# Optimization experiments

Hardware: AMD Instinct MI355X
Metric: run time of the kernel (lower is better)

The kernel has to match this reference:

```python
import jax, jax.numpy as jnp
import numpy as np

H = 768      # hidden_size
NH = 12      # num_heads
HD = H // NH # head_dim = 64


def setup_inputs() -> dict:
    key = jax.random.key(0)
    k1, k2, k3 = jax.random.split(key, 3)
    x = jax.random.normal(k1, (4, 2048, H), dtype=jnp.float32)
    # nn.Linear weights are [out, in]; we store transposed [in, out] for x @ W
    w_qkv = jax.random.normal(k2, (H, 3 * H), dtype=jnp.float32) * (1.0 / np.sqrt(H))
    w_out = jax.random.normal(k3, (H, H), dtype=jnp.float32) * (1.0 / np.sqrt(H))
    return {"x": x, "w_qkv": w_qkv, "w_out": w_out}


def reference(x, w_qkv, w_out):
    B, S, _ = x.shape
    qkv = (x @ w_qkv).reshape(B, S, 3, NH, HD)
    qkv = jnp.transpose(qkv, (2, 0, 3, 1, 4))  # [3, B, NH, S, HD]
    q, k, v = qkv[0], qkv[1], qkv[2]
    scale = 1.0 / np.sqrt(HD)
    scores = jnp.einsum('bhqd,bhkd->bhqk', q, k) * scale  # [B,NH,S,S]
    causal = jnp.tril(jnp.ones((S, S), dtype=bool))
    scores = jnp.where(causal, scores, jnp.finfo(scores.dtype).min)
    attn = jax.nn.softmax(scores, axis=-1)
    out = jnp.einsum('bhqk,bhkd->bhqd', attn, v)          # [B,NH,S,HD]
    out = jnp.transpose(out, (0, 2, 1, 3)).reshape(B, S, H)
    return out @ w_out
```

## Files before the change

kernel.cpp:

```cpp
#include <hip/hip_runtime.h>
#include <type_traits>

#define S_LEN 2048
#define HID   768
#define NHEAD 12
#define HDIM  64
#define BATCH 4

typedef __attribute__((ext_vector_type(4))) float float4v;
typedef __attribute__((ext_vector_type(8))) short short8;
typedef __attribute__((ext_vector_type(4))) short short4v;
typedef __attribute__((ext_vector_type(2))) int int2v;

__device__ __forceinline__ short f2b(float f) {
  unsigned u = __float_as_uint(f);
  u += 0x7fff + ((u >> 16) & 1);
  return (short)(u >> 16);
}

__device__ __forceinline__ unsigned pkbf(float a, float b) {
#if __has_builtin(__builtin_amdgcn_cvt_pk_bf16_f32)
  typedef __attribute__((ext_vector_type(2))) __bf16 bf2;
  bf2 r = __builtin_amdgcn_cvt_pk_bf16_f32(a, b);
  return *(unsigned*)&r;
#else
  return ((unsigned)(unsigned short)f2b(a)) |
         (((unsigned)(unsigned short)f2b(b)) << 16);
#endif
}

__device__ __forceinline__ float fexp2(float x) {
#if __has_builtin(__builtin_amdgcn_exp2f)
  return __builtin_amdgcn_exp2f(x);
#else
  return __expf(x * 0.69314718056f);
#endif
}

__device__ __forceinline__ void g2l16(const short* g, short* l) {
  __builtin_amdgcn_global_load_lds(
      (const __attribute__((address_space(1))) void*)g,
      (__attribute__((address_space(3))) void*)l, 16, 0, 0);
}

__global__ __launch_bounds__(256) void prepass(const float* __restrict__ x,
                                               const float* __restrict__ w_qkv,
                                               const float* __restrict__ w_out,
                                               short* __restrict__ xb,
                                               short* __restrict__ wqkvT,
                                               short* __restrict__ woutT) {
  __shared__ float tile[64][65];
  const int blk = blockIdx.x;
  if (blk < 3072) {
    int i = blk * 2048 + threadIdx.x * 8;
    float4v a = *(const float4v*)&x[i];
    float4v b = *(const float4v*)&x[i + 4];
    short8 o;
#pragma unroll
    for (int j = 0; j < 4; j++) { o[j] = f2b(a[j]); o[j + 4] = f2b(b[j]); }
    *(short8*)&xb[i] = o;
    return;
  }
  const float* W; short* WT; int N_, scaleN, idx;
  if (blk < 3504) { idx = blk - 3072; W = w_qkv; WT = wqkvT; N_ = 3 * HID; scaleN = HID; }
  else            { idx = blk - 3504; W = w_out; WT = woutT; N_ = HID;     scaleN = 0;  }
  const int nblk = N_ / 64;
  const int n0 = (idx % nblk) * 64, k0 = (idx / nblk) * 64;
  const int tx = threadIdx.x & 63, ty = threadIdx.x >> 6;
#pragma unroll
  for (int r = 0; r < 16; r++) {
    int row = r * 4 + ty;
    tile[row][tx] = W[(size_t)(k0 + row) * N_ + n0 + tx];
  }
  __syncthreads();
#pragma unroll
  for (int r = 0; r < 16; r++) {
    int row = r * 4 + ty;
    float sc = (n0 + row < scaleN) ? 0.18033688011f : 1.0f;
    WT[(size_t)(n0 + row) * HID + k0 + tx] = f2b(tile[tx][row] * sc);
  }
}

template <int OUT>
__global__ __launch_bounds__(256) void gemm_bt(const short* __restrict__ A,
                                               const short* __restrict__ Bt,
                                               float* __restrict__ Cf,
                                               short* __restrict__ Cq,
                                               short* __restrict__ vT,
                                               int M, int N, int K) {
  __shared__ __align__(16) short As[2][128 * 32];
  __shared__ __align__(16) short Bs[2][128 * 32];
  const int tid = threadIdx.x;
  const int w = tid >> 6, lane = tid & 63;
  const int quad = lane >> 4, lm = lane & 15;

  const int gx = gridDim.x;
  const int nwg = gx * gridDim.y;
  int flat = blockIdx.y * gx + blockIdx.x;
  if ((nwg & 7) == 0) flat = (flat & 7) * (nwg >> 3) + (flat >> 3);
  const int m0 = (flat / gx) * 128, n0 = (flat % gx) * 128;
  const int mo = (w & 1) * 64, no = (w >> 1) * 64;

  float4v acc[4][4];
#pragma unroll
  for (int i = 0; i < 4; i++)
#pragma unroll
    for (int j = 0; j < 4; j++) acc[i][j] = (float4v)0.0f;

  const int srow = w * 32 + (lane >> 2);
  const int scol = ((lane & 3) ^ ((lane >> 3) & 3)) * 8;
  const short* Ag = A + (size_t)(m0 + srow) * K + scol;
  const short* Bg = Bt + (size_t)(n0 + srow) * K + scol;

  const int qsw8 = (quad ^ ((lm >> 1) & 3)) * 8;

  for (int kb = 0; kb < K; kb += 64) {
#pragma unroll
    for (int s = 0; s < 2; s++) {
      short* Al = &As[s][(w * 32) * 32];
      short* Bl = &Bs[s][(w * 32) * 32];
      g2l16(Ag + kb + s * 32, Al);
      g2l16(Ag + kb + s * 32 + (size_t)16 * K, Al + 16 * 32);
      g2l16(Bg + kb + s * 32, Bl);
      g2l16(Bg + kb + s * 32 + (size_t)16 * K, Bl + 16 * 32);
    }
    __syncthreads();

#pragma unroll
    for (int s = 0; s < 2; s++) {
      short8 af[4], bf[4];
#pragma unroll
      for (int i = 0; i < 4; i++)
        af[i] = *(const short8*)&As[s][(mo + i * 16 + lm) * 32 + qsw8];
#pragma unroll
      for (int j = 0; j < 4; j++)
        bf[j] = *(const short8*)&Bs[s][(no + j * 16 + lm) * 32 + qsw8];
#pragma unroll
      for (int i = 0; i < 4; i++)
#pragma unroll
        for (int j = 0; j < 4; j++) {
          if constexpr (OUT == 2)
            acc[i][j] = __builtin_amdgcn_mfma_f32_16x16x32_bf16(bf[j], af[i], acc[i][j], 0, 0, 0);
          else
            acc[i][j] = __builtin_amdgcn_mfma_f32_16x16x32_bf16(af[i], bf[j], acc[i][j], 0, 0, 0);
        }
    }
    __syncthreads();
  }

  if constexpr (OUT == 0) {
#pragma unroll
    for (int i = 0; i < 4; i++)
#pragma unroll
      for (int j = 0; j < 4; j++)
#pragma unroll
        for (int r = 0; r < 4; r++)
          Cf[(size_t)(m0 + mo + i * 16 + quad * 4 + r) * N + n0 + no + j * 16 + lm] =
              acc[i][j][r];
  } else if constexpr (OUT == 1) {
#pragma unroll
    for (int i = 0; i < 4; i++)
#pragma unroll
      for (int j = 0; j < 4; j++)
#pragma unroll
        for (int r = 0; r < 4; r++)
          Cq[(size_t)(m0 + mo + i * 16 + quad * 4 + r) * (2 * HID) + n0 + no + j * 16 + lm] =
              f2b(acc[i][j][r]);
  } else {
    const int b = m0 >> 11;
#pragma unroll
    for (int i = 0; i < 4; i++) {
      const int sG = (m0 & 2047) + mo + i * 16 + lm;
#pragma unroll
      for (int j = 0; j < 4; j++) {
#pragma unroll
        for (int r = 0; r < 4; r++) {
          int col = n0 + no + j * 16 + quad * 4 + r;
          int h = col >> 6, d = col & 63;
          vT[((size_t)(b * NHEAD + h) * HDIM + d) * S_LEN + sG] = f2b(acc[i][j][r]);
        }
      }
    }
  }
}

__global__ __launch_bounds__(256) void attn_mfma(const short* __restrict__ qk,
                                                 const short* __restrict__ vT,
                                                 short* __restrict__ attnout) {
  __shared__ __align__(16) short Ks[2][64 * 64];
  __shared__ __align__(16) short Vt[2][64 * 64];
  __shared__ __align__(16) short Ps[4][16 * 64];

  const int tid = threadIdx.x;
  const int w = tid >> 6, lane = tid & 63;
  const int quad = lane >> 4, lm = lane & 15;
  const int bh = blockIdx.x, a = blockIdx.y;
  const int b = bh / NHEAD, h = bh % NHEAD;
  const int qtile[2] = {a, 31 - a};

  short8 aq[2][2];
#pragma unroll
  for (int t = 0; t < 2; t++)
#pragma unroll
    for (int kb = 0; kb < 2; kb++)
      aq[t][kb] = *(const short8*)&qk[(size_t)(b * S_LEN + qtile[t] * 64 + w * 16 + lm) * (2 * HID) +
                                      h * HDIM + kb * 32 + quad * 8];

  const float4v z4 = (float4v)0.0f;
  short8 one8;
#pragma unroll
  for (int j = 0; j < 8; j++) one8[j] = (short)0x3F80;

  const size_t kbase = (size_t)(b * S_LEN) * (2 * HID) + HID + h * HDIM;
  const size_t vbase = (size_t)(b * NHEAD + h) * HDIM * S_LEN;
  const short* kptr[2];
  const short* vptr[2];
#pragma unroll
  for (int i = 0; i < 2; i++) {
    int c = (w * 2 + i) * 64 + lane;
    int row = c >> 3, slot = c & 7;
    int q8 = slot ^ (row & 7);
    int key = 4 * (row & 15) + (row >> 4);
    kptr[i] = qk + kbase + (size_t)key * (2 * HID) + q8 * 8;
    vptr[i] = vT + vbase + (size_t)row * S_LEN + q8 * 8;
  }

#define ISSUE(BUF)                                                    \
  {                                                                   \
    _Pragma("unroll") for (int i = 0; i < 2; i++) {                   \
      g2l16(kptr[i], &Ks[BUF][(w * 2 + i) * 512]);                    \
      g2l16(vptr[i], &Vt[BUF][(w * 2 + i) * 512]);                    \
      kptr[i] += 64 * 2 * HID;                                        \
      vptr[i] += 64;                                                  \
    }                                                                 \
  }

  const int swx = (lm & 7) << 4;
  const int loff0 = (quad * 16) ^ swx;
  const int loff1 = (64 + quad * 16) ^ swx;
  const int rowK = lm << 7;
  const char* KsB = (const char*)&Ks[0][0];
  const char* VtB = (const char*)&Vt[0][0];
  const char* PsW = (const char*)&Ps[w][0];
  const char* pread0 = PsW + rowK + loff0;
  const char* pread1 = PsW + rowK + loff1;
  char* pswa[4];
#pragma unroll
  for (int r = 0; r < 4; r++) {
    int rowp = quad * 4 + r;
    pswa[r] = (char*)PsW + (rowp << 7) + ((lm * 8) ^ ((rowp & 7) << 4));
  }

  float4v o_acc[2][4];
#pragma unroll
  for (int t = 0; t < 2; t++)
#pragma unroll
    for (int nt = 0; nt < 4; nt++) o_acc[t][nt] = (float4v)0.0f;
  float4v o1[2];
  o1[0] = (float4v)0.0f;
  o1[1] = (float4v)0.0f;

  const int ktmax = 32 - a;
  int cur = 0;

  ISSUE(0);

  for (int kt = 0; kt < ktmax; kt++) {
    asm volatile("s_waitcnt vmcnt(0)" ::: "memory");
    __syncthreads();
    if (kt + 1 < ktmax) ISSUE(cur ^ 1);

    const int coff = cur << 13;
    const char* kB0 = KsB + coff + rowK + loff0;
    const char* kB1 = KsB + coff + rowK + loff1;
    const char* vB0 = VtB + coff + rowK + loff0;
    const char* vB1 = VtB + coff + rowK + loff1;

#pragma unroll
    for (int t = 0; t < 2; t++) {
      if (t == 0 && kt > a) continue;
      float4v s_acc[4];
      __builtin_amdgcn_s_setprio(1);
#pragma unroll
      for (int nt = 0; nt < 4; nt++) {
        short8 bk = *(const short8*)(kB0 + nt * 2048);
        s_acc[nt] = __builtin_amdgcn_mfma_f32_16x16x32_bf16(aq[t][0], bk, z4, 0, 0, 0);
      }
#pragma unroll
      for (int nt = 0; nt < 4; nt++) {
        short8 bk = *(const short8*)(kB1 + nt * 2048);
        s_acc[nt] = __builtin_amdgcn_mfma_f32_16x16x32_bf16(aq[t][1], bk, s_acc[nt], 0, 0, 0);
      }
      __builtin_amdgcn_s_setprio(0);

      const bool diag = (kt == qtile[t]);
#pragma unroll
      for (int r = 0; r < 4; r++) {
        float e[4];
#pragma unroll
        for (int nt = 0; nt < 4; nt++) {
          float v = fexp2(s_acc[nt][r]);
          if (diag && (4 * lm + nt > w * 16 + quad * 4 + r)) v = 0.0f;
          e[nt] = v;
        }
        int2v p2 = {(int)pkbf(e[0], e[1]), (int)pkbf(e[2], e[3])};
        *(int2v*)pswa[r] = p2;
      }

      __builtin_amdgcn_s_setprio(1);
#pragma unroll
      for (int kb = 0; kb < 2; kb++) {
        short8 ap = *(const short8*)(kb ? pread1 : pread0);
        const char* vB = kb ? vB1 : vB0;
        o1[t] = __builtin_amdgcn_mfma_f32_16x16x32_bf16(ap, one8, o1[t], 0, 0, 0);
#pragma unroll
        for (int nt = 0; nt < 4; nt++) {
          short8 bv = *(const short8*)(vB + nt * 2048);
          o_acc[t][nt] = __builtin_amdgcn_mfma_f32_16x16x32_bf16(ap, bv, o_acc[t][nt], 0, 0, 0);
        }
      }
      __builtin_amdgcn_s_setprio(0);
    }
    cur ^= 1;
  }

#pragma unroll
  for (int t = 0; t < 2; t++)
#pragma unroll
    for (int r = 0; r < 4; r++) {
      float inv = 1.0f / o1[t][r];
      int rowg = b * S_LEN + qtile[t] * 64 + w * 16 + quad * 4 + r;
#pragma unroll
      for (int nt = 0; nt < 4; nt++)
        attnout[(size_t)rowg * HID + h * HDIM + nt * 16 + lm] =
            f2b(o_acc[t][nt][r] * inv);
    }
#undef ISSUE
}

extern "C" void kernel_launch(void* const* d_in, const int* in_sizes, int n_in,
                              void* d_out, int out_size, void* d_ws, size_t ws_size,
                              hipStream_t stream) {
  const float* x     = (const float*)d_in[0];
  const float* w_qkv = (const float*)d_in[1];
  const float* w_out = (const float*)d_in[2];
  float* out = (float*)d_out;

  const int M = BATCH * S_LEN;
  short* qk     = (short*)d_ws;
  short* attn   = qk + (size_t)M * 2 * HID;
  short* vT     = attn + (size_t)M * HID;
  short* xb     = vT + (size_t)M * HID;
  short* wqkvT  = xb + (size_t)M * HID;
  short* woutT  = wqkvT + (size_t)(3 * HID) * HID;

  prepass<<<3648, 256, 0, stream>>>(x, w_qkv, w_out, xb, wqkvT, woutT);

  gemm_bt<1><<<dim3(2 * HID / 128, M / 128), 256, 0, stream>>>(
      xb, wqkvT, nullptr, qk, nullptr, M, 2 * HID, HID);
  gemm_bt<2><<<dim3(HID / 128, M / 128), 256, 0, stream>>>(
      xb, wqkvT + (size_t)(2 * HID) * HID, nullptr, nullptr, vT, M, HID, HID);
  attn_mfma<<<dim3(BATCH * NHEAD, S_LEN / 128), 256, 0, stream>>>(qk, vT, attn);
  gemm_bt<0><<<dim3(HID / 128, M / 128), 256, 0, stream>>>(
      attn, woutT, out, nullptr, nullptr, M, HID, HID);
}
```

Baseline: 194.4 us.

## Split paired causal query tiles into one tile per block, longest first

The attention kernel previously paired query tile a with tile 31-a in each block, sharing each K/V tile load across both query tiles for load balance. Now each block handles a single 64-row query tile, and launch order goes from the longest tile down (qt = 31 - blockIdx.y). This doubles the grid to 1536 blocks, raising occupancy and parallelism and lowering per-thread register pressure. In exchange, each K/V tile is loaded separately for each query tile, roughly doubling K/V traffic and synchronisation per unit of work.

```diff
diff --git a/kernel.cpp b/kernel.cpp
--- a/kernel.cpp
+++ b/kernel.cpp
@@ -194,17 +194,15 @@
   const int tid = threadIdx.x;
   const int w = tid >> 6, lane = tid & 63;
   const int quad = lane >> 4, lm = lane & 15;
-  const int bh = blockIdx.x, a = blockIdx.y;
+  const int bh = blockIdx.x;
+  const int qt = 31 - blockIdx.y;
   const int b = bh / NHEAD, h = bh % NHEAD;
-  const int qtile[2] = {a, 31 - a};
-
-  short8 aq[2][2];
-#pragma unroll
-  for (int t = 0; t < 2; t++)
-#pragma unroll
-    for (int kb = 0; kb < 2; kb++)
-      aq[t][kb] = *(const short8*)&qk[(size_t)(b * S_LEN + qtile[t] * 64 + w * 16 + lm) * (2 * HID) +
-                                      h * HDIM + kb * 32 + quad * 8];
+
+  short8 aq[2];
+#pragma unroll
+  for (int kb = 0; kb < 2; kb++)
+    aq[kb] = *(const short8*)&qk[(size_t)(b * S_LEN + qt * 64 + w * 16 + lm) * (2 * HID) +
+                                 h * HDIM + kb * 32 + quad * 8];
 
   const float4v z4 = (float4v)0.0f;
   short8 one8;
@@ -251,16 +249,12 @@
     pswa[r] = (char*)PsW + (rowp << 7) + ((lm * 8) ^ ((rowp & 7) << 4));
   }
 
-  float4v o_acc[2][4];
-#pragma unroll
-  for (int t = 0; t < 2; t++)
-#pragma unroll
-    for (int nt = 0; nt < 4; nt++) o_acc[t][nt] = (float4v)0.0f;
-  float4v o1[2];
-  o1[0] = (float4v)0.0f;
-  o1[1] = (float4v)0.0f;
-
-  const int ktmax = 32 - a;
+  float4v o_acc[4];
+#pragma unroll
+  for (int nt = 0; nt < 4; nt++) o_acc[nt] = (float4v)0.0f;
+  float4v o1 = (float4v)0.0f;
+
+  const int ktmax = qt + 1;
   int cur = 0;
 
   ISSUE(0);
@@ -276,65 +270,60 @@
     const char* vB0 = VtB + coff + rowK + loff0;
     const char* vB1 = VtB + coff + rowK + loff1;
 
-#pragma unroll
-    for (int t = 0; t < 2; t++) {
-      if (t == 0 && kt > a) continue;
-      float4v s_acc[4];
-      __builtin_amdgcn_s_setprio(1);
+    float4v s_acc[4];
+    __builtin_amdgcn_s_setprio(1);
+#pragma unroll
+    for (int nt = 0; nt < 4; nt++) {
+      short8 bk = *(const short8*)(kB0 + nt * 2048);
+      s_acc[nt] = __builtin_amdgcn_mfma_f32_16x16x32_bf16(aq[0], bk, z4, 0, 0, 0);
+    }
+#pragma unroll
+    for (int nt = 0; nt < 4; nt++) {
+      short8 bk = *(const short8*)(kB1 + nt * 2048);
+      s_acc[nt] = __builtin_amdgcn_mfma_f32_16x16x32_bf16(aq[1], bk, s_acc[nt], 0, 0, 0);
+    }
+    __builtin_amdgcn_s_setprio(0);
+
+    const bool diag = (kt == qt);
+#pragma unroll
+    for (int r = 0; r < 4; r++) {
+      float e[4];
 #pragma unroll
       for (int nt = 0; nt < 4; nt++) {
-        short8 bk = *(const short8*)(kB0 + nt * 2048);
-        s_acc[nt] = __builtin_amdgcn_mfma_f32_16x16x32_bf16(aq[t][0], bk, z4, 0, 0, 0);
+        float v = fexp2(s_acc[nt][r]);
+        if (diag && (4 * lm + nt > w * 16 + quad * 4 + r)) v = 0.0f;
+        e[nt] = v;
       }
+      int2v p2 = {(int)pkbf(e[0], e[1]), (int)pkbf(e[2], e[3])};
+      *(int2v*)pswa[r] = p2;
+    }
+
+    __builtin_amdgcn_s_setprio(1);
+#pragma unroll
+    for (int kb = 0; kb < 2; kb++) {
+      short8 ap = *(const short8*)(kb ? pread1 : pread0);
+      const char* vB = kb ? vB1 : vB0;
+      o1 = __builtin_amdgcn_mfma_f32_16x16x32_bf16(ap, one8, o1, 0, 0, 0);
 #pragma unroll
       for (int nt = 0; nt < 4; nt++) {
-        short8 bk = *(const short8*)(kB1 + nt * 2048);
-        s_acc[nt] = __builtin_amdgcn_mfma_f32_16x16x32_bf16(aq[t][1], bk, s_acc[nt], 0, 0, 0);
+        short8 bv = *(const short8*)(vB + nt * 2048);
+        o_acc[nt] = __builtin_amdgcn_mfma_f32_16x16x32_bf16(ap, bv, o_acc[nt], 0, 0, 0);
       }
-      __builtin_amdgcn_s_setprio(0);
-
-      const bool diag = (kt == qtile[t]);
-#pragma unroll
-      for (int r = 0; r < 4; r++) {
-        float e[4];
-#pragma unroll
-        for (int nt = 0; nt < 4; nt++) {
-          float v = fexp2(s_acc[nt][r]);
-          if (diag && (4 * lm + nt > w * 16 + quad * 4 + r)) v = 0.0f;
-          e[nt] = v;
-        }
-        int2v p2 = {(int)pkbf(e[0], e[1]), (int)pkbf(e[2], e[3])};
-        *(int2v*)pswa[r] = p2;
-      }
-
-      __builtin_amdgcn_s_setprio(1);
-#pragma unroll
-      for (int kb = 0; kb < 2; kb++) {
-        short8 ap = *(const short8*)(kb ? pread1 : pread0);
-        const char* vB = kb ? vB1 : vB0;
-        o1[t] = __builtin_amdgcn_mfma_f32_16x16x32_bf16(ap, one8, o1[t], 0, 0, 0);
-#pragma unroll
-        for (int nt = 0; nt < 4; nt++) {
-          short8 bv = *(const short8*)(vB + nt * 2048);
-          o_acc[t][nt] = __builtin_amdgcn_mfma_f32_16x16x32_bf16(ap, bv, o_acc[t][nt], 0, 0, 0);
-        }
-      }
-      __builtin_amdgcn_s_setprio(0);
-    }
+    }
+    __builtin_amdgcn_s_setprio(0);
+
     cur ^= 1;
   }
 
 #pragma unroll
-  for (int t = 0; t < 2; t++)
-#pragma unroll
-    for (int r = 0; r < 4; r++) {
-      float inv = 1.0f / o1[t][r];
-      int rowg = b * S_LEN + qtile[t] * 64 + w * 16 + quad * 4 + r;
-#pragma unroll
-      for (int nt = 0; nt < 4; nt++)
-        attnout[(size_t)rowg * HID + h * HDIM + nt * 16 + lm] =
-            f2b(o_acc[t][nt][r] * inv);
-    }
+  for (int r = 0; r < 4; r++) {
+    float inv = 1.0f / o1[r];
+    int rowg = b * S_LEN + qt * 64 + w * 16 + quad * 4 + r;
+#pragma unroll
+    for (int nt = 0; nt < 4; nt++)
+      attnout[(size_t)rowg * HID + h * HDIM + nt * 16 + lm] =
+          f2b(o_acc[nt][r] * inv);
+  }
 #undef ISSUE
 }
 
@@ -360,7 +349,7 @@
       xb, wqkvT, nullptr, qk, nullptr, M, 2 * HID, HID);
   gemm_bt<2><<<dim3(HID / 128, M / 128), 256, 0, stream>>>(
       xb, wqkvT + (size_t)(2 * HID) * HID, nullptr, nullptr, vT, M, HID, HID);
-  attn_mfma<<<dim3(BATCH * NHEAD, S_LEN / 128), 256, 0, stream>>>(qk, vT, attn);
+  attn_mfma<<<dim3(BATCH * NHEAD, 32), 256, 0, stream>>>(qk, vT, attn);
   gemm_bt<0><<<dim3(HID / 128, M / 128), 256, 0, stream>>>(
       attn, woutT, out, nullptr, nullptr, M, HID, HID);
 }
```

Measured after the change: 196.2 us. About the same (+1.0%).
